# Kernel tuning notes

Measured on AMD Instinct MI355X. Metric: run time of the kernel, lower is better.

## Reference

```python
import jax, jax.numpy as jnp
import numpy as np

B, S, E = 2, 2048, 1024
H, D = 16, 64
BASE = 10000.0


def rotate_half(x):
    x1, x2 = jnp.split(x, 2, axis=-1)
    return jnp.concatenate((-x2, x1), axis=-1)


def rope_cos_sin(seq_len, dim):
    inv_freq = 1.0 / (BASE ** (jnp.arange(0, dim, 2, dtype=jnp.float32) / dim))
    t = jnp.arange(seq_len, dtype=jnp.float32)
    freqs = jnp.einsum('i,j->ij', t, inv_freq)          # [S, D/2]
    emb = jnp.concatenate((freqs, freqs), axis=-1)       # [S, D]
    return jnp.cos(emb), jnp.sin(emb)


def setup_inputs() -> dict:
    key = jax.random.key(0)
    ks = jax.random.split(key, 9)
    s = 1.0 / np.sqrt(E)
    inp = {
        'x': jax.random.normal(ks[0], (B, S, E), dtype=jnp.float32),
        'mask': jnp.ones((B, S), dtype=jnp.int32),
        'Wq': jax.random.normal(ks[1], (E, H * D), dtype=jnp.float32) * s,
        'bq': jnp.zeros((H * D,), dtype=jnp.float32),
        'Wk': jax.random.normal(ks[2], (E, H * D), dtype=jnp.float32) * s,
        'bk': jnp.zeros((H * D,), dtype=jnp.float32),
        'Wv': jax.random.normal(ks[3], (E, H * D), dtype=jnp.float32) * s,
        'bv': jnp.zeros((H * D,), dtype=jnp.float32),
        'Wo': jax.random.normal(ks[4], (H * D, E), dtype=jnp.float32) * s,
        'bo': jnp.zeros((E,), dtype=jnp.float32),
    }
    return inp


def reference(x, mask, Wq, bq, Wk, bk, Wv, bv, Wo, bo):
    b, s, _ = x.shape
    scale = D ** (-0.5)
    # projections -> [B, H, S, D]
    q = (x @ Wq + bq).reshape(b, s, H, D).transpose(0, 2, 1, 3)
    k = (x @ Wk + bk).reshape(b, s, H, D).transpose(0, 2, 1, 3)
    v = (x @ Wv + bv).reshape(b, s, H, D).transpose(0, 2, 1, 3)
    # rotary position embedding
    cos, sin = rope_cos_sin(s, D)                      # [S, D]
    cos = cos[None, None]
    sin = sin[None, None]
    q = q * cos + rotate_half(q) * sin
    k = k * cos + rotate_half(k) * sin
    # scores [B, H, S, S]
    scores = jnp.einsum('bhqd,bhkd->bhqk', q, k) * scale
    # padding mask [B,1,1,S]
    scores = jnp.where(mask[:, None, None, :] == 0, -jnp.inf, scores)
    # causal mask
    i = jnp.arange(s)
    causal = jnp.where(i[None, :] > i[:, None], -jnp.inf, 0.0)  # [S, S]
    scores = scores + causal[None, None]
    attn = jax.nn.softmax(scores, axis=-1)
    ctx = jnp.einsum('bhqk,bhkd->bhqd', attn, v)
    ctx = ctx.transpose(0, 2, 1, 3).reshape(b, s, H * D)
    return ctx @ Wo + bo
```

## Files before the change

### kernel.cpp

```cpp
#include <hip/hip_runtime.h>
#include <cstdint>
#include <cstddef>

#define DEVI __device__ __forceinline__

typedef __bf16 bf16_t;
typedef __bf16 bf16x4 __attribute__((ext_vector_type(4)));
typedef __bf16 bf16x8 __attribute__((ext_vector_type(8)));
typedef float  f32x4  __attribute__((ext_vector_type(4)));
typedef unsigned short u16x4 __attribute__((ext_vector_type(4)));

static constexpr int Bz = 2, S = 2048, E = 1024, H = 16, Dh = 64;
static constexpr int M  = Bz * S;
static constexpr int N  = H * Dh;
static constexpr int Kd = E;

DEVI unsigned short f2bf(float f) {
  unsigned u = __builtin_bit_cast(unsigned, f);
  return (unsigned short)((u + 0x7fffu + ((u >> 16) & 1u)) >> 16);
}

DEVI void async_copy16(void* lds, const void* g) {
  __builtin_amdgcn_global_load_lds((__attribute__((address_space(1))) void*)(g),
                                   (__attribute__((address_space(3))) void*)(lds), 16, 0, 0);
}

__global__ void prep_kernel(const float* __restrict__ x, bf16_t* __restrict__ xb,
                            const float* __restrict__ Wq, const float* __restrict__ Wk,
                            const float* __restrict__ Wv, const float* __restrict__ Wo,
                            bf16_t* __restrict__ WtBase,
                            float* __restrict__ ropeC, float* __restrict__ ropeS) {
  __shared__ unsigned short tile[64][68];
  const int blk = blockIdx.x, tid = threadIdx.x;
  if (blk < 4096) {
    int i = blk * 256 + tid;
    float4 v = ((const float4*)x)[i];
    u16x4 o = { f2bf(v.x), f2bf(v.y), f2bf(v.z), f2bf(v.w) };
    ((u16x4*)xb)[i] = o;
  } else if (blk < 5120) {
    const int i = blk - 4096;
    const int z = i >> 8, rest = i & 255;
    const int n0 = (rest & 15) * 64, k0 = (rest >> 4) * 64;
    const float* W = (z == 0) ? Wq : (z == 1) ? Wk : (z == 2) ? Wv : Wo;
    unsigned short* T = (unsigned short*)(WtBase + (size_t)z * Kd * N);
    for (int e = tid; e < 1024; e += 256) {
      int r = e >> 4, c4 = (e & 15) * 4;
      float4 v = *(const float4*)(W + (size_t)(k0 + r) * N + n0 + c4);
      u16x4 o = { f2bf(v.x), f2bf(v.y), f2bf(v.z), f2bf(v.w) };
      *(u16x4*)&tile[r][c4] = o;
    }
    __syncthreads();
    for (int e = tid; e < 1024; e += 256) {
      int r = e >> 4, c4 = (e & 15) * 4;
      u16x4 o = { tile[c4][r], tile[c4 + 1][r], tile[c4 + 2][r], tile[c4 + 3][r] };
      *(u16x4*)&T[(size_t)(n0 + r) * Kd + k0 + c4] = o;
    }
  } else {
    int i = (blk - 5120) * 256 + tid;
    int pos = i >> 5, j = i & 31;
    float inv = exp2f(-(float)j * 0.41524101186092029f);
    float ang = (float)pos * inv;
    ropeC[i] = cosf(ang);
    ropeS[i] = sinf(ang);
  }
}

__global__ void vtrans_kernel(const bf16_t* __restrict__ V, bf16_t* __restrict__ Vt) {
  __shared__ unsigned short tile[64][68];
  const int bh = blockIdx.y;
  const int s0 = blockIdx.x * 64;
  const unsigned short* Vp = (const unsigned short*)V + (size_t)bh * S * Dh;
  unsigned short* Tp = (unsigned short*)Vt + (size_t)bh * Dh * S;
  const int tid = threadIdx.x;
  for (int e = tid; e < 1024; e += 256) {
    int r = e >> 4, c4 = (e & 15) * 4;
    u16x4 v = *(const u16x4*)(Vp + (size_t)(s0 + r) * Dh + c4);
    *(u16x4*)&tile[r][c4] = v;
  }
  __syncthreads();
  for (int e = tid; e < 1024; e += 256) {
    int d = e >> 4, s4 = (e & 15) * 4;
    u16x4 o = { tile[s4][d], tile[s4 + 1][d], tile[s4 + 2][d], tile[s4 + 3][d] };
    *(u16x4*)&Tp[(size_t)d * S + s0 + s4] = o;
  }
}


DEVI void gemm_mainloop(const bf16_t* __restrict__ A, const bf16_t* __restrict__ Bt,
                        bf16_t* sA, bf16_t* sB, int m0, int n0, f32x4 (&acc)[4][4]) {
  const int tid  = threadIdx.x;
  const int lane = tid & 63;
  const int wid  = tid >> 6;
  const int l16  = lane & 15;
  const int quad = lane >> 4;
  const int wm = (wid >> 1) * 64;
  const int wn = (wid & 1) * 64;
  const int o0 = wid * 2048 + lane * 16;
  const int o1 = o0 + 1024;
  const int r0 = o0 >> 6, c0 = o0 & 63;
  const int r1 = o1 >> 6, c1 = o1 & 63;
  const char* Ab = (const char*)A;
  const char* Bb = (const char*)Bt;
  char* sAc = (char*)sA;
  char* sBc = (char*)sB;

  for (int k0 = 0; k0 < Kd; k0 += 32) {
    __syncthreads();
    async_copy16(sAc + wid * 2048,        Ab + ((size_t)(m0 + r0) * Kd + k0) * 2 + c0);
    async_copy16(sAc + wid * 2048 + 1024, Ab + ((size_t)(m0 + r1) * Kd + k0) * 2 + c1);
    async_copy16(sBc + wid * 2048,        Bb + ((size_t)(n0 + r0) * Kd + k0) * 2 + c0);
    async_copy16(sBc + wid * 2048 + 1024, Bb + ((size_t)(n0 + r1) * Kd + k0) * 2 + c1);
    __syncthreads();
    bf16x8 af[4], bfv[4];
#pragma unroll
    for (int mi = 0; mi < 4; ++mi)
      af[mi] = *(const bf16x8*)(sA + (wm + mi * 16 + l16) * 32 + quad * 8);
#pragma unroll
    for (int ni = 0; ni < 4; ++ni)
      bfv[ni] = *(const bf16x8*)(sB + (wn + ni * 16 + l16) * 32 + quad * 8);
#pragma unroll
    for (int mi = 0; mi < 4; ++mi)
#pragma unroll
      for (int ni = 0; ni < 4; ++ni)
        acc[mi][ni] = __builtin_amdgcn_mfma_f32_16x16x32_bf16(af[mi], bfv[ni], acc[mi][ni], 0, 0, 0);
  }
}

__global__ __launch_bounds__(256, 3) void gemm_qkv_kernel(
    const bf16_t* __restrict__ xb, const bf16_t* __restrict__ WtBase,
    const float* __restrict__ bq, const float* __restrict__ bk, const float* __restrict__ bv,
    bf16_t* __restrict__ outBase,
    const float* __restrict__ ropeC, const float* __restrict__ ropeS) {
  __shared__ bf16_t sA[4096], sB[4096];
  const int z = blockIdx.z;
  const bf16_t* Bt = WtBase + (size_t)z * Kd * N;
  const float* bias = (z == 0) ? bq : (z == 1) ? bk : bv;
  unsigned short* outp = (unsigned short*)(outBase + (size_t)z * M * N);
  const int n0 = blockIdx.x * 128, m0 = blockIdx.y * 128;
  f32x4 acc[4][4] = {};
  gemm_mainloop(xb, Bt, sA, sB, m0, n0, acc);

  const int tid = threadIdx.x, lane = tid & 63, wid = tid >> 6;
  const int l16 = lane & 15, quad = lane >> 4;
  const int wm = (wid >> 1) * 64, wn = (wid & 1) * 64;
  const int cbase = n0 + wn;
  const int h = cbase >> 6;

  if (z < 2) {
    const float qs = (z == 0) ? 0.18033688011112042f : 1.0f;
#pragma unroll
    for (int mi = 0; mi < 4; ++mi)
#pragma unroll
      for (int r = 0; r < 4; ++r) {
        int t = m0 + wm + mi * 16 + quad * 4 + r;
        int bb = t >> 11, s = t & (S - 1);
        size_t obase = ((size_t)(bb * H + h) * S + s) * Dh;
#pragma unroll
        for (int np = 0; np < 2; ++np) {
          int j = np * 16 + l16;
          float cc = ropeC[s * 32 + j];
          float ss = ropeS[s * 32 + j];
          float xlo = acc[mi][np][r]     + bias[cbase + j];
          float xhi = acc[mi][np + 2][r] + bias[cbase + j + 32];
          outp[obase + j]      = f2bf((xlo * cc - xhi * ss) * qs);
          outp[obase + j + 32] = f2bf((xhi * cc + xlo * ss) * qs);
        }
      }
  } else {
#pragma unroll
    for (int mi = 0; mi < 4; ++mi)
#pragma unroll
      for (int r = 0; r < 4; ++r) {
        int t = m0 + wm + mi * 16 + quad * 4 + r;
        int bb = t >> 11, s = t & (S - 1);
        size_t obase = ((size_t)(bb * H + h) * S + s) * Dh;
#pragma unroll
        for (int ni = 0; ni < 4; ++ni) {
          int d = ni * 16 + l16;
          outp[obase + d] = f2bf(acc[mi][ni][r] + bias[cbase + d]);
        }
      }
  }
}

__global__ __launch_bounds__(256, 4) void gemm_o_kernel(
    const bf16_t* __restrict__ A, const bf16_t* __restrict__ Bt,
    const float* __restrict__ bias, float* __restrict__ out) {
  __shared__ bf16_t sA[2048], sB[4096];
  const int n0 = blockIdx.x * 128, m0 = blockIdx.y * 64;
  const int tid = threadIdx.x, lane = tid & 63, wid = tid >> 6;
  const int l16 = lane & 15, quad = lane >> 4;
  const int wm = (wid >> 1) * 32, wn = (wid & 1) * 64;
  const int rowoff = lane >> 2, col8 = (lane & 3) * 8;
  const char* Ab = (const char*)A;
  const char* Bb = (const char*)Bt;
  char* sAc = (char*)sA;
  char* sBc = (char*)sB;
  f32x4 acc[2][4] = {};

  for (int k0 = 0; k0 < Kd; k0 += 32) {
    __syncthreads();
    async_copy16(sAc + wid * 1024,
                 Ab + ((size_t)(m0 + wid * 16 + rowoff) * Kd + k0 + col8) * 2);
    async_copy16(sBc + (wid * 2) * 1024,
                 Bb + ((size_t)(n0 + wid * 32 + rowoff) * Kd + k0 + col8) * 2);
    async_copy16(sBc + (wid * 2 + 1) * 1024,
                 Bb + ((size_t)(n0 + wid * 32 + 16 + rowoff) * Kd + k0 + col8) * 2);
    __syncthreads();
    bf16x8 af[2], bfv[4];
#pragma unroll
    for (int mi = 0; mi < 2; ++mi)
      af[mi] = *(const bf16x8*)(sA + (wm + mi * 16 + l16) * 32 + quad * 8);
#pragma unroll
    for (int ni = 0; ni < 4; ++ni)
      bfv[ni] = *(const bf16x8*)(sB + (wn + ni * 16 + l16) * 32 + quad * 8);
#pragma unroll
    for (int mi = 0; mi < 2; ++mi)
#pragma unroll
      for (int ni = 0; ni < 4; ++ni)
        acc[mi][ni] = __builtin_amdgcn_mfma_f32_16x16x32_bf16(af[mi], bfv[ni], acc[mi][ni], 0, 0, 0);
  }
#pragma unroll
  for (int mi = 0; mi < 2; ++mi)
#pragma unroll
    for (int r = 0; r < 4; ++r) {
      int t = m0 + wm + mi * 16 + quad * 4 + r;
#pragma unroll
      for (int ni = 0; ni < 4; ++ni) {
        int c = n0 + wn + ni * 16 + l16;
        out[(size_t)t * N + c] = acc[mi][ni][r] + bias[c];
      }
    }
}

__global__ __launch_bounds__(256, 3) void attn_kernel(
    const bf16_t* __restrict__ Q, const bf16_t* __restrict__ Kb,
    const bf16_t* __restrict__ Vt, const int* __restrict__ mask,
    bf16_t* __restrict__ ctx) {
  __shared__ bf16_t sK[8192];
  __shared__ bf16_t sV[8192];
  __shared__ unsigned short sP[4][16 * 136];

  const int tid = threadIdx.x, lane = tid & 63, wid = tid >> 6;
  const int l16 = lane & 15, quad = lane >> 4;

  const int idx = blockIdx.x;
  const int qb  = 31 - (idx >> 5);
  const int bh  = idx & 31;
  const int b   = bh >> 4;
  const int q0  = qb * 64;
  const int qw  = q0 + wid * 16;

  const bf16_t* Qp = Q + ((size_t)bh * S + qw) * Dh;
  const char*   Kg = (const char*)(Kb + (size_t)bh * S * Dh);
  const char*   Vg = (const char*)(Vt + (size_t)bh * Dh * S);
  const int*    mp = mask + b * S;

  bf16x8 qf0 = *(const bf16x8*)(Qp + l16 * Dh + quad * 8);
  bf16x8 qf1 = *(const bf16x8*)(Qp + l16 * Dh + 32 + quad * 8);

  int    sLds[4];
  size_t kGo[4], vGo[4];
#pragma unroll
  for (int i = 0; i < 4; ++i) {
    int sk = wid * 4 + i;
    int g = sk >> 1, c = sk & 1;
    sLds[i] = sk * 1024;
    kGo[i] = ((size_t)(g * 16 + l16) * Dh + c * 32 + quad * 8) * 2;
    vGo[i] = ((size_t)(wid * 16 + l16) * S + i * 32 + quad * 8) * 2;
  }
  char* sKc = (char*)sK;
  char* sVc = (char*)sV;

  f32x4 acc[4] = {};
  float lsum = 0.f;
  const int qcol = qw + l16;
  const int niter = (qb >> 1) + 1;
  unsigned short* pb = &sP[wid][0];

  for (int kt = 0; kt < niter; ++kt) {
    const int kb = kt * 128;
    __syncthreads();
#pragma unroll
    for (int i = 0; i < 4; ++i) {
      async_copy16(sKc + sLds[i], Kg + (size_t)kb * (Dh * 2) + kGo[i]);
      async_copy16(sVc + sLds[i], Vg + (size_t)kb * 2 + vGo[i]);
    }
    int mk0 = mp[kb + lane];
    int mk1 = mp[kb + 64 + lane];
    __syncthreads();

    f32x4 st[8];
#pragma unroll
    for (int g = 0; g < 8; ++g) {
      bf16x8 kf0 = *(const bf16x8*)(sK + (g * 2 + 0) * 512 + lane * 8);
      bf16x8 kf1 = *(const bf16x8*)(sK + (g * 2 + 1) * 512 + lane * 8);
      f32x4 z = {};
      z = __builtin_amdgcn_mfma_f32_16x16x32_bf16(kf0, qf0, z, 0, 0, 0);
      z = __builtin_amdgcn_mfma_f32_16x16x32_bf16(kf1, qf1, z, 0, 0, 0);
      st[g] = z;
    }

    unsigned long long dm0 = __ballot(mk0 == 0);
    unsigned long long dm1 = __ballot(mk1 == 0);
    if (dm0 | dm1) {
#pragma unroll
      for (int g = 0; g < 8; ++g) {
        unsigned long long dm = (g < 4) ? dm0 : dm1;
#pragma unroll
        for (int r = 0; r < 4; ++r)
          if ((dm >> ((g & 3) * 16 + quad * 4 + r)) & 1ull) st[g][r] = -1e30f;
      }
    }
    if (kt == niter - 1) {
#pragma unroll
      for (int g = 0; g < 8; ++g)
#pragma unroll
        for (int r = 0; r < 4; ++r)
          if (kb + g * 16 + quad * 4 + r > qcol) st[g][r] = -1e30f;
    }

#pragma unroll
    for (int g = 0; g < 8; ++g) {
      float e0 = exp2f(st[g][0]), e1 = exp2f(st[g][1]);
      float e2 = exp2f(st[g][2]), e3 = exp2f(st[g][3]);
      lsum += (e0 + e1) + (e2 + e3);
      bf16x4 pk = { (bf16_t)e0, (bf16_t)e1, (bf16_t)e2, (bf16_t)e3 };
      *(bf16x4*)&pb[l16 * 136 + g * 16 + quad * 4] = pk;
    }
    bf16x8 pf[4];
#pragma unroll
    for (int kc = 0; kc < 4; ++kc)
      pf[kc] = *(const bf16x8*)((const bf16_t*)(const void*)pb + l16 * 136 + kc * 32 + quad * 8);

#pragma unroll
    for (int dt = 0; dt < 4; ++dt)
#pragma unroll
      for (int kc = 0; kc < 4; ++kc) {
        bf16x8 vf = *(const bf16x8*)(sV + (dt * 4 + kc) * 512 + lane * 8);
        acc[dt] = __builtin_amdgcn_mfma_f32_16x16x32_bf16(vf, pf[kc], acc[dt], 0, 0, 0);
      }
  }

  lsum += __shfl_xor(lsum, 16);
  lsum += __shfl_xor(lsum, 32);
  float inv = 1.0f / lsum;
  unsigned short* cp = (unsigned short*)ctx;
  size_t trow = ((size_t)(b * S + qw + l16)) * N + (size_t)(bh & 15) * Dh;
#pragma unroll
  for (int dt = 0; dt < 4; ++dt) {
    u16x4 o = { f2bf(acc[dt][0] * inv), f2bf(acc[dt][1] * inv),
                f2bf(acc[dt][2] * inv), f2bf(acc[dt][3] * inv) };
    *(u16x4*)&cp[trow + dt * 16 + quad * 4] = o;
  }
}


extern "C" void kernel_launch(void* const* d_in, const int* in_sizes, int n_in,
                              void* d_out, int out_size, void* d_ws, size_t ws_size,
                              hipStream_t stream) {
  const float* x  = (const float*)d_in[0];
  const int*  msk = (const int*)d_in[1];
  const float* Wq = (const float*)d_in[2];
  const float* bq = (const float*)d_in[3];
  const float* Wk = (const float*)d_in[4];
  const float* bk = (const float*)d_in[5];
  const float* Wv = (const float*)d_in[6];
  const float* bv = (const float*)d_in[7];
  const float* Wo = (const float*)d_in[8];
  const float* bo = (const float*)d_in[9];
  float* out = (float*)d_out;
  (void)in_sizes; (void)n_in; (void)out_size; (void)ws_size;

  char* ws = (char*)d_ws;
  bf16_t* xb   = (bf16_t*)(ws);
  bf16_t* WT   = (bf16_t*)(ws + (8u  << 20));
  bf16_t* qkv  = (bf16_t*)(ws + (16u << 20));
  bf16_t* Qb   = qkv;
  bf16_t* Kbuf = qkv + (size_t)1 * M * N;
  bf16_t* Vb   = qkv + (size_t)2 * M * N;
  bf16_t* Vt   = xb;
  bf16_t* ctx  = Vb;
  float* ropeC = (float*)(ws + (40u << 20));
  float* ropeS = ropeC + (size_t)S * 32;

  prep_kernel<<<5376, 256, 0, stream>>>(x, xb, Wq, Wk, Wv, Wo, WT, ropeC, ropeS);
  gemm_qkv_kernel<<<dim3(8, 32, 3), 256, 0, stream>>>(xb, WT, bq, bk, bv, qkv, ropeC, ropeS);
  vtrans_kernel<<<dim3(32, 32), 256, 0, stream>>>(Vb, Vt);
  attn_kernel<<<1024, 256, 0, stream>>>(Qb, Kbuf, Vt, msk, ctx);
  gemm_o_kernel<<<dim3(8, 64), 256, 0, stream>>>(ctx, WT + (size_t)3 * Kd * N, bo, out);
}
```

Before: 197.8 us.

## Pair causal query blocks per CTA with double-buffered K/V and mask fast path

Each attention block now handles two query tiles (j and 31-j) that share K/V tiles, which balances causal work and halves the grid. K/V loads are double-buffered with explicit vmcnt waits and raw barriers, so the next tile's global-to-LDS copy overlaps compute. A one-time mask scan chooses a template path that skips per-tile mask loads and ballots when no positions are padded. It also adds an XOR swizzle on the P scratch buffer and setprio around MFMA sections. In exchange, LDS use doubles and occupancy drops to 2 blocks per CU.

After: 204.1 us. 3.2% more time.

```diff
diff --git a/kernel.cpp b/kernel.cpp
--- a/kernel.cpp
+++ b/kernel.cpp
@@ -24,6 +24,9 @@
   __builtin_amdgcn_global_load_lds((__attribute__((address_space(1))) void*)(g),
                                    (__attribute__((address_space(3))) void*)(lds), 16, 0, 0);
 }
+
+#define VMCNT8() asm volatile("s_waitcnt vmcnt(8)" ::: "memory")
+#define VMCNT0() asm volatile("s_waitcnt vmcnt(0)" ::: "memory")
 
 __global__ void prep_kernel(const float* __restrict__ x, bf16_t* __restrict__ xb,
                             const float* __restrict__ Wq, const float* __restrict__ Wk,
@@ -233,126 +236,220 @@
     }
 }
 
-__global__ __launch_bounds__(256, 3) void attn_kernel(
+template <bool MASKED>
+DEVI void attn_body(const bf16_t* __restrict__ Qp, const char* __restrict__ Kg,
+                    const char* __restrict__ Vg, const int* __restrict__ mp,
+                    unsigned short* __restrict__ cp, char* sKc, char* sVc,
+                    unsigned short* __restrict__ pb, int b, int bh,
+                    int qbS, int qbL) {
+  const int tid = threadIdx.x, lane = tid & 63, wid = tid >> 6;
+  const int l16 = lane & 15, quad = lane >> 4;
+  const int nS = (qbS >> 1) + 1, nL = (qbL >> 1) + 1;
+  const int qwS = qbS * 64 + wid * 16, qwL = qbL * 64 + wid * 16;
+  const int qcS = qwS + l16, qcL = qwL + l16;
+  const int swz = (l16 & 7) << 4;
+
+  bf16x8 qSf0 = *(const bf16x8*)(Qp + (size_t)(qwS + l16) * Dh + quad * 8);
+  bf16x8 qSf1 = *(const bf16x8*)(Qp + (size_t)(qwS + l16) * Dh + 32 + quad * 8);
+  bf16x8 qLf0 = *(const bf16x8*)(Qp + (size_t)(qwL + l16) * Dh + quad * 8);
+  bf16x8 qLf1 = *(const bf16x8*)(Qp + (size_t)(qwL + l16) * Dh + 32 + quad * 8);
+
+  int sLds[4], kGo[4], vGo[4];
+#pragma unroll
+  for (int i = 0; i < 4; ++i) {
+    int sk = wid * 4 + i, g = sk >> 1, c = sk & 1;
+    sLds[i] = sk * 1024;
+    kGo[i] = ((g * 16 + l16) * Dh + c * 32 + quad * 8) * 2;
+    vGo[i] = ((wid * 16 + l16) * S + i * 32 + quad * 8) * 2;
+  }
+
+  f32x4 accL[4] = {}, accS[4] = {};
+  float lsumL = 0.f, lsumS = 0.f;
+
+#pragma unroll
+  for (int i = 0; i < 4; ++i) {
+    async_copy16(sKc + sLds[i], Kg + kGo[i]);
+    async_copy16(sVc + sLds[i], Vg + vGo[i]);
+  }
+
+  for (int kt = 0; kt < nL; ++kt) {
+    const int cur = kt & 1;
+    const int kb = kt * 128;
+    if (kt + 1 < nL) {
+      const char* Kn = Kg + (size_t)(kb + 128) * (Dh * 2);
+      const char* Vn = Vg + (size_t)(kb + 128) * 2;
+      char* kd = sKc + (cur ^ 1) * 16384;
+      char* vd = sVc + (cur ^ 1) * 16384;
+#pragma unroll
+      for (int i = 0; i < 4; ++i) {
+        async_copy16(kd + sLds[i], Kn + kGo[i]);
+        async_copy16(vd + sLds[i], Vn + vGo[i]);
+      }
+      if (!MASKED) { VMCNT8(); }
+    } else if (!MASKED) {
+      VMCNT0();
+    }
+    int mk0 = 0, mk1 = 0;
+    if (MASKED) {
+      mk0 = mp[kb + lane];
+      mk1 = mp[kb + 64 + lane];
+      VMCNT0();
+    }
+    __builtin_amdgcn_s_barrier();
+
+    const bf16_t* sKt = (const bf16_t*)(sKc + cur * 16384);
+    const bf16_t* sVt = (const bf16_t*)(sVc + cur * 16384);
+    const bool doS = kt < nS;
+
+    f32x4 stL[8], stS[8];
+    __builtin_amdgcn_s_setprio(1);
+#pragma unroll
+    for (int g = 0; g < 8; ++g) {
+      bf16x8 kf0 = *(const bf16x8*)(sKt + (g * 2 + 0) * 512 + lane * 8);
+      bf16x8 kf1 = *(const bf16x8*)(sKt + (g * 2 + 1) * 512 + lane * 8);
+      f32x4 z = {};
+      z = __builtin_amdgcn_mfma_f32_16x16x32_bf16(kf0, qLf0, z, 0, 0, 0);
+      z = __builtin_amdgcn_mfma_f32_16x16x32_bf16(kf1, qLf1, z, 0, 0, 0);
+      stL[g] = z;
+      if (doS) {
+        f32x4 y = {};
+        y = __builtin_amdgcn_mfma_f32_16x16x32_bf16(kf0, qSf0, y, 0, 0, 0);
+        y = __builtin_amdgcn_mfma_f32_16x16x32_bf16(kf1, qSf1, y, 0, 0, 0);
+        stS[g] = y;
+      }
+    }
+    __builtin_amdgcn_s_setprio(0);
+
+    if (MASKED) {
+      unsigned long long dm0 = __ballot(mk0 == 0);
+      unsigned long long dm1 = __ballot(mk1 == 0);
+      if (dm0 | dm1) {
+#pragma unroll
+        for (int g = 0; g < 8; ++g) {
+          unsigned long long dm = (g < 4) ? dm0 : dm1;
+#pragma unroll
+          for (int r = 0; r < 4; ++r)
+            if ((dm >> ((g & 3) * 16 + quad * 4 + r)) & 1ull) {
+              stL[g][r] = -1e30f;
+              if (doS) stS[g][r] = -1e30f;
+            }
+        }
+      }
+    }
+    if (kt == nL - 1) {
+#pragma unroll
+      for (int g = 0; g < 8; ++g)
+#pragma unroll
+        for (int r = 0; r < 4; ++r)
+          if (kb + g * 16 + quad * 4 + r > qcL) stL[g][r] = -1e30f;
+    }
+    if (doS && kt == nS - 1) {
+#pragma unroll
+      for (int g = 0; g < 8; ++g)
+#pragma unroll
+        for (int r = 0; r < 4; ++r)
+          if (kb + g * 16 + quad * 4 + r > qcS) stS[g][r] = -1e30f;
+    }
+
+#pragma unroll
+    for (int g = 0; g < 8; ++g) {
+      float e0 = exp2f(stL[g][0]), e1 = exp2f(stL[g][1]);
+      float e2 = exp2f(stL[g][2]), e3 = exp2f(stL[g][3]);
+      lsumL += (e0 + e1) + (e2 + e3);
+      bf16x4 pk = { (bf16_t)e0, (bf16_t)e1, (bf16_t)e2, (bf16_t)e3 };
+      *(bf16x4*)((char*)pb + ((l16 * 256 + g * 32 + quad * 8) ^ swz)) = pk;
+    }
+    {
+      bf16x8 pf[4];
+#pragma unroll
+      for (int kc = 0; kc < 4; ++kc)
+        pf[kc] = *(const bf16x8*)((const char*)pb + ((l16 * 256 + kc * 64 + quad * 16) ^ swz));
+      __builtin_amdgcn_s_setprio(1);
+#pragma unroll
+      for (int dt = 0; dt < 4; ++dt)
+#pragma unroll
+        for (int kc = 0; kc < 4; ++kc) {
+          bf16x8 vf = *(const bf16x8*)(sVt + (dt * 4 + kc) * 512 + lane * 8);
+          accL[dt] = __builtin_amdgcn_mfma_f32_16x16x32_bf16(vf, pf[kc], accL[dt], 0, 0, 0);
+        }
+      __builtin_amdgcn_s_setprio(0);
+    }
+    if (doS) {
+#pragma unroll
+      for (int g = 0; g < 8; ++g) {
+        float e0 = exp2f(stS[g][0]), e1 = exp2f(stS[g][1]);
+        float e2 = exp2f(stS[g][2]), e3 = exp2f(stS[g][3]);
+        lsumS += (e0 + e1) + (e2 + e3);
+        bf16x4 pk = { (bf16_t)e0, (bf16_t)e1, (bf16_t)e2, (bf16_t)e3 };
+        *(bf16x4*)((char*)pb + ((l16 * 256 + g * 32 + quad * 8) ^ swz)) = pk;
+      }
+      bf16x8 pf[4];
+#pragma unroll
+      for (int kc = 0; kc < 4; ++kc)
+        pf[kc] = *(const bf16x8*)((const char*)pb + ((l16 * 256 + kc * 64 + quad * 16) ^ swz));
+      __builtin_amdgcn_s_setprio(1);
+#pragma unroll
+      for (int dt = 0; dt < 4; ++dt)
+#pragma unroll
+        for (int kc = 0; kc < 4; ++kc) {
+          bf16x8 vf = *(const bf16x8*)(sVt + (dt * 4 + kc) * 512 + lane * 8);
+          accS[dt] = __builtin_amdgcn_mfma_f32_16x16x32_bf16(vf, pf[kc], accS[dt], 0, 0, 0);
+        }
+      __builtin_amdgcn_s_setprio(0);
+    }
+    __builtin_amdgcn_s_barrier();
+  }
+
+  lsumL += __shfl_xor(lsumL, 16); lsumL += __shfl_xor(lsumL, 32);
+  lsumS += __shfl_xor(lsumS, 16); lsumS += __shfl_xor(lsumS, 32);
+  const float invL = 1.0f / lsumL, invS = 1.0f / lsumS;
+  const size_t trL = ((size_t)(b * S + qwL + l16)) * N + (size_t)(bh & 15) * Dh;
+  const size_t trS = ((size_t)(b * S + qwS + l16)) * N + (size_t)(bh & 15) * Dh;
+#pragma unroll
+  for (int dt = 0; dt < 4; ++dt) {
+    u16x4 oL = { f2bf(accL[dt][0] * invL), f2bf(accL[dt][1] * invL),
+                 f2bf(accL[dt][2] * invL), f2bf(accL[dt][3] * invL) };
+    *(u16x4*)&cp[trL + dt * 16 + quad * 4] = oL;
+    u16x4 oS = { f2bf(accS[dt][0] * invS), f2bf(accS[dt][1] * invS),
+                 f2bf(accS[dt][2] * invS), f2bf(accS[dt][3] * invS) };
+    *(u16x4*)&cp[trS + dt * 16 + quad * 4] = oS;
+  }
+}
+
+__global__ __launch_bounds__(256, 2) void attn_kernel(
     const bf16_t* __restrict__ Q, const bf16_t* __restrict__ Kb,
     const bf16_t* __restrict__ Vt, const int* __restrict__ mask,
     bf16_t* __restrict__ ctx) {
-  __shared__ bf16_t sK[8192];
-  __shared__ bf16_t sV[8192];
-  __shared__ unsigned short sP[4][16 * 136];
-
-  const int tid = threadIdx.x, lane = tid & 63, wid = tid >> 6;
-  const int l16 = lane & 15, quad = lane >> 4;
+  __shared__ bf16_t sK[2][8192];
+  __shared__ bf16_t sV[2][8192];
+  __shared__ unsigned short sP[4][2048];
 
   const int idx = blockIdx.x;
-  const int qb  = 31 - (idx >> 5);
-  const int bh  = idx & 31;
-  const int b   = bh >> 4;
-  const int q0  = qb * 64;
-  const int qw  = q0 + wid * 16;
-
-  const bf16_t* Qp = Q + ((size_t)bh * S + qw) * Dh;
+  const int j  = idx >> 5;
+  const int bh = idx & 31;
+  const int b  = bh >> 4;
+  const int lane = threadIdx.x & 63, wid = threadIdx.x >> 6;
+
+  const bf16_t* Qp = Q + (size_t)bh * S * Dh;
   const char*   Kg = (const char*)(Kb + (size_t)bh * S * Dh);
   const char*   Vg = (const char*)(Vt + (size_t)bh * Dh * S);
   const int*    mp = mask + b * S;
 
-  bf16x8 qf0 = *(const bf16x8*)(Qp + l16 * Dh + quad * 8);
-  bf16x8 qf1 = *(const bf16x8*)(Qp + l16 * Dh + 32 + quad * 8);
-
-  int    sLds[4];
-  size_t kGo[4], vGo[4];
-#pragma unroll
-  for (int i = 0; i < 4; ++i) {
-    int sk = wid * 4 + i;
-    int g = sk >> 1, c = sk & 1;
-    sLds[i] = sk * 1024;
-    kGo[i] = ((size_t)(g * 16 + l16) * Dh + c * 32 + quad * 8) * 2;
-    vGo[i] = ((size_t)(wid * 16 + l16) * S + i * 32 + quad * 8) * 2;
-  }
-  char* sKc = (char*)sK;
-  char* sVc = (char*)sV;
-
-  f32x4 acc[4] = {};
-  float lsum = 0.f;
-  const int qcol = qw + l16;
-  const int niter = (qb >> 1) + 1;
-  unsigned short* pb = &sP[wid][0];
-
-  for (int kt = 0; kt < niter; ++kt) {
-    const int kb = kt * 128;
-    __syncthreads();
-#pragma unroll
-    for (int i = 0; i < 4; ++i) {
-      async_copy16(sKc + sLds[i], Kg + (size_t)kb * (Dh * 2) + kGo[i]);
-      async_copy16(sVc + sLds[i], Vg + (size_t)kb * 2 + vGo[i]);
-    }
-    int mk0 = mp[kb + lane];
-    int mk1 = mp[kb + 64 + lane];
-    __syncthreads();
-
-    f32x4 st[8];
-#pragma unroll
-    for (int g = 0; g < 8; ++g) {
-      bf16x8 kf0 = *(const bf16x8*)(sK + (g * 2 + 0) * 512 + lane * 8);
-      bf16x8 kf1 = *(const bf16x8*)(sK + (g * 2 + 1) * 512 + lane * 8);
-      f32x4 z = {};
-      z = __builtin_amdgcn_mfma_f32_16x16x32_bf16(kf0, qf0, z, 0, 0, 0);
-      z = __builtin_amdgcn_mfma_f32_16x16x32_bf16(kf1, qf1, z, 0, 0, 0);
-      st[g] = z;
-    }
-
-    unsigned long long dm0 = __ballot(mk0 == 0);
-    unsigned long long dm1 = __ballot(mk1 == 0);
-    if (dm0 | dm1) {
-#pragma unroll
-      for (int g = 0; g < 8; ++g) {
-        unsigned long long dm = (g < 4) ? dm0 : dm1;
-#pragma unroll
-        for (int r = 0; r < 4; ++r)
-          if ((dm >> ((g & 3) * 16 + quad * 4 + r)) & 1ull) st[g][r] = -1e30f;
-      }
-    }
-    if (kt == niter - 1) {
-#pragma unroll
-      for (int g = 0; g < 8; ++g)
-#pragma unroll
-        for (int r = 0; r < 4; ++r)
-          if (kb + g * 16 + quad * 4 + r > qcol) st[g][r] = -1e30f;
-    }
-
-#pragma unroll
-    for (int g = 0; g < 8; ++g) {
-      float e0 = exp2f(st[g][0]), e1 = exp2f(st[g][1]);
-      float e2 = exp2f(st[g][2]), e3 = exp2f(st[g][3]);
-      lsum += (e0 + e1) + (e2 + e3);
-      bf16x4 pk = { (bf16_t)e0, (bf16_t)e1, (bf16_t)e2, (bf16_t)e3 };
-      *(bf16x4*)&pb[l16 * 136 + g * 16 + quad * 4] = pk;
-    }
-    bf16x8 pf[4];
-#pragma unroll
-    for (int kc = 0; kc < 4; ++kc)
-      pf[kc] = *(const bf16x8*)((const bf16_t*)(const void*)pb + l16 * 136 + kc * 32 + quad * 8);
-
-#pragma unroll
-    for (int dt = 0; dt < 4; ++dt)
-#pragma unroll
-      for (int kc = 0; kc < 4; ++kc) {
-        bf16x8 vf = *(const bf16x8*)(sV + (dt * 4 + kc) * 512 + lane * 8);
-        acc[dt] = __builtin_amdgcn_mfma_f32_16x16x32_bf16(vf, pf[kc], acc[dt], 0, 0, 0);
-      }
-  }
-
-  lsum += __shfl_xor(lsum, 16);
-  lsum += __shfl_xor(lsum, 32);
-  float inv = 1.0f / lsum;
+  int dead = 0;
+  const int4* mp4 = (const int4*)mp;
+  for (int c = lane; c < S / 4; c += 64) {
+    int4 m = mp4[c];
+    dead |= (m.x == 0) | (m.y == 0) | (m.z == 0) | (m.w == 0);
+  }
+  const bool anydead = __ballot(dead != 0) != 0ull;
+
   unsigned short* cp = (unsigned short*)ctx;
-  size_t trow = ((size_t)(b * S + qw + l16)) * N + (size_t)(bh & 15) * Dh;
-#pragma unroll
-  for (int dt = 0; dt < 4; ++dt) {
-    u16x4 o = { f2bf(acc[dt][0] * inv), f2bf(acc[dt][1] * inv),
-                f2bf(acc[dt][2] * inv), f2bf(acc[dt][3] * inv) };
-    *(u16x4*)&cp[trow + dt * 16 + quad * 4] = o;
-  }
+  if (!anydead)
+    attn_body<false>(Qp, Kg, Vg, mp, cp, (char*)&sK[0][0], (char*)&sV[0][0],
+                     &sP[wid][0], b, bh, j, 31 - j);
+  else
+    attn_body<true>(Qp, Kg, Vg, mp, cp, (char*)&sK[0][0], (char*)&sV[0][0],
+                    &sP[wid][0], b, bh, j, 31 - j);
 }
 
 
@@ -387,6 +484,6 @@
   prep_kernel<<<5376, 256, 0, stream>>>(x, xb, Wq, Wk, Wv, Wo, WT, ropeC, ropeS);
   gemm_qkv_kernel<<<dim3(8, 32, 3), 256, 0, stream>>>(xb, WT, bq, bk, bv, qkv, ropeC, ropeS);
   vtrans_kernel<<<dim3(32, 32), 256, 0, stream>>>(Vb, Vt);
-  attn_kernel<<<1024, 256, 0, stream>>>(Qb, Kbuf, Vt, msk, ctx);
+  attn_kernel<<<512, 256, 0, stream>>>(Qb, Kbuf, Vt, msk, ctx);
   gemm_o_kernel<<<dim3(8, 64), 256, 0, stream>>>(ctx, WT + (size_t)3 * Kd * N, bo, out);
 }
```

## Rewrite attention with 32x32 MFMA, split-K warp groups and double-buffered K/V

Applied to the files above, without the earlier changes.

The attention kernel now runs 512-thread blocks over 128-query tiles, split into two warp groups that each cover half of the key range and combine their partial sums through LDS at the end. It uses 32x32x16 MFMAs and builds the P operand in registers with cvt_pk and permlane32 swaps instead of a round trip through LDS. K/V tiles are double-buffered with async global-to-LDS copies. A block-wide mask precheck selects a template path that skips per-tile mask loads when nothing is masked. The scheduling is more complex and raises register/LDS pressure, and the query tiles are ordered to balance causal work.

Measured after the change: 196.1 us. Within noise of the previous version (-0.8%).

```diff
diff --git a/kernel.cpp b/kernel.cpp
--- a/kernel.cpp
+++ b/kernel.cpp
@@ -8,7 +8,9 @@
 typedef __bf16 bf16x4 __attribute__((ext_vector_type(4)));
 typedef __bf16 bf16x8 __attribute__((ext_vector_type(8)));
 typedef float  f32x4  __attribute__((ext_vector_type(4)));
+typedef float  f32x16 __attribute__((ext_vector_type(16)));
 typedef unsigned short u16x4 __attribute__((ext_vector_type(4)));
+typedef unsigned int   u32x4 __attribute__((ext_vector_type(4)));
 
 static constexpr int Bz = 2, S = 2048, E = 1024, H = 16, Dh = 64;
 static constexpr int M  = Bz * S;
@@ -23,6 +25,19 @@
 DEVI void async_copy16(void* lds, const void* g) {
   __builtin_amdgcn_global_load_lds((__attribute__((address_space(1))) void*)(g),
                                    (__attribute__((address_space(3))) void*)(lds), 16, 0, 0);
+}
+
+DEVI void block_sync() { asm volatile("s_barrier" ::: "memory"); }
+#define VMCNT4() asm volatile("s_waitcnt vmcnt(4)" ::: "memory")
+#define VMCNT0() asm volatile("s_waitcnt vmcnt(0)" ::: "memory")
+
+DEVI unsigned cvtpk(float lo, float hi) {
+  unsigned r;
+  asm("v_cvt_pk_bf16_f32 %0, %1, %2" : "=v"(r) : "v"(lo), "v"(hi));
+  return r;
+}
+DEVI void swap32(unsigned& x, unsigned& y) {
+  asm("v_permlane32_swap_b32 %0, %1" : "+v"(x), "+v"(y));
 }
 
 __global__ void prep_kernel(const float* __restrict__ x, bf16_t* __restrict__ xb,
@@ -233,126 +248,192 @@
     }
 }
 
-__global__ __launch_bounds__(256, 3) void attn_kernel(
+template <bool MASKED>
+DEVI void attn32_body(const bf16_t* __restrict__ Qp, const char* __restrict__ Kg,
+                      const char* __restrict__ Vg, const int* __restrict__ mp,
+                      unsigned short* __restrict__ cp, char* lds,
+                      int b, int bh, int qb) {
+  const int tid = threadIdx.x, lane = tid & 63, wid = tid >> 6;
+  const int grp = wid >> 2, w4 = wid & 3;
+  const int l32 = lane & 31, hi = lane >> 5;
+
+  const int qw = qb * 128 + w4 * 32;
+  const int qg = qw + l32;
+  const int nIt = qb + 1;
+  const int gk0 = grp * nIt * 64;
+  char* gB = lds + grp * 32768;
+
+  bf16x8 qf[4];
+#pragma unroll
+  for (int c = 0; c < 4; ++c)
+    qf[c] = *(const bf16x8*)(Qp + (size_t)(qw + l32) * Dh + c * 16 + hi * 8);
+  asm volatile("" :: "v"((float)qf[3][7]));
+
+  int kLds[2], vLds[2], kOff[2], vOff[2];
+#pragma unroll
+  for (int i = 0; i < 2; ++i) {
+    const int s = w4 * 2 + i;
+    const int a = s >> 2, c = s & 3;
+    kLds[i] = s * 1024;
+    kOff[i] = ((a * 32 + l32) * Dh + c * 16 + hi * 8) * 2;
+    vLds[i] = 8192 + s * 1024;
+    vOff[i] = ((s >> 2) * 32 + l32) * (S * 2) + (((s & 3) * 16 + hi * 8) * 2);
+  }
+
+  f32x16 cacc0 = {}, cacc1 = {};
+  float lsum = 0.f;
+
+  {
+    const char* ks = Kg + (size_t)gk0 * (Dh * 2);
+    const char* vs = Vg + (size_t)gk0 * 2;
+    async_copy16(gB + kLds[0], ks + kOff[0]);
+    async_copy16(gB + kLds[1], ks + kOff[1]);
+    async_copy16(gB + vLds[0], vs + vOff[0]);
+    async_copy16(gB + vLds[1], vs + vOff[1]);
+  }
+
+  for (int kt = 0; kt < nIt; ++kt) {
+    const int cur = kt & 1;
+    const int kb = gk0 + kt * 64;
+    if (kt + 1 < nIt) {
+      char* dst = gB + (cur ^ 1) * 16384;
+      const char* ks = Kg + (size_t)(kb + 64) * (Dh * 2);
+      const char* vs = Vg + (size_t)(kb + 64) * 2;
+      async_copy16(dst + kLds[0], ks + kOff[0]);
+      async_copy16(dst + kLds[1], ks + kOff[1]);
+      async_copy16(dst + vLds[0], vs + vOff[0]);
+      async_copy16(dst + vLds[1], vs + vOff[1]);
+      if (!MASKED) { VMCNT4(); }
+    } else if (!MASKED) {
+      VMCNT0();
+    }
+    unsigned long long dm = 0;
+    if (MASKED) {
+      int mk = mp[kb + lane];
+      VMCNT0();
+      dm = __ballot(mk == 0);
+    }
+    block_sync();
+
+    const bf16_t* sK = (const bf16_t*)(gB + cur * 16384);
+    const bf16_t* sV = (const bf16_t*)(gB + cur * 16384 + 8192);
+    const bool needC = (kb + 63 > qw);
+
+#pragma unroll
+    for (int a = 0; a < 2; ++a) {
+      f32x16 st = {};
+      __builtin_amdgcn_s_setprio(1);
+#pragma unroll
+      for (int c = 0; c < 4; ++c) {
+        bf16x8 kf = *(const bf16x8*)(sK + (a * 4 + c) * 512 + lane * 8);
+        st = __builtin_amdgcn_mfma_f32_32x32x16_bf16(kf, qf[c], st, 0, 0, 0);
+      }
+      __builtin_amdgcn_s_setprio(0);
+      if (MASKED && dm) {
+#pragma unroll
+        for (int r = 0; r < 16; ++r)
+          if ((dm >> (a * 32 + (r & 3) + 8 * (r >> 2) + 4 * hi)) & 1ull) st[r] = -1e30f;
+      }
+      if (needC) {
+        const int kbase = kb + a * 32 + 4 * hi - qg;
+#pragma unroll
+        for (int r = 0; r < 16; ++r)
+          if (kbase + (r & 3) + 8 * (r >> 2) > 0) st[r] = -1e30f;
+      }
+      unsigned P0[4], P1[4];
+#pragma unroll
+      for (int m = 0; m < 4; ++m) {
+        float p0 = exp2f(st[4 * m + 0]), p1 = exp2f(st[4 * m + 1]);
+        float p2 = exp2f(st[4 * m + 2]), p3 = exp2f(st[4 * m + 3]);
+        lsum += (p0 + p1) + (p2 + p3);
+        P0[m] = cvtpk(p0, p1);
+        P1[m] = cvtpk(p2, p3);
+      }
+      swap32(P0[0], P0[1]); swap32(P1[0], P1[1]);
+      swap32(P0[2], P0[3]); swap32(P1[2], P1[3]);
+      u32x4 t0 = { P0[0], P1[0], P0[1], P1[1] };
+      u32x4 t1 = { P0[2], P1[2], P0[3], P1[3] };
+      const bf16x8 f0 = __builtin_bit_cast(bf16x8, t0);
+      const bf16x8 f1 = __builtin_bit_cast(bf16x8, t1);
+      __builtin_amdgcn_s_setprio(1);
+      {
+        bf16x8 v00 = *(const bf16x8*)(sV + (0 + a * 2 + 0) * 512 + lane * 8);
+        cacc0 = __builtin_amdgcn_mfma_f32_32x32x16_bf16(v00, f0, cacc0, 0, 0, 0);
+        bf16x8 v01 = *(const bf16x8*)(sV + (0 + a * 2 + 1) * 512 + lane * 8);
+        cacc0 = __builtin_amdgcn_mfma_f32_32x32x16_bf16(v01, f1, cacc0, 0, 0, 0);
+        bf16x8 v10 = *(const bf16x8*)(sV + (4 + a * 2 + 0) * 512 + lane * 8);
+        cacc1 = __builtin_amdgcn_mfma_f32_32x32x16_bf16(v10, f0, cacc1, 0, 0, 0);
+        bf16x8 v11 = *(const bf16x8*)(sV + (4 + a * 2 + 1) * 512 + lane * 8);
+        cacc1 = __builtin_amdgcn_mfma_f32_32x32x16_bf16(v11, f1, cacc1, 0, 0, 0);
+      }
+      __builtin_amdgcn_s_setprio(0);
+    }
+    block_sync();
+  }
+
+  float* cm = (float*)lds + (size_t)w4 * 2112;
+  if (grp == 1) {
+#pragma unroll
+    for (int r = 0; r < 16; ++r) cm[r * 64 + lane] = cacc0[r];
+#pragma unroll
+    for (int r = 0; r < 16; ++r) cm[(16 + r) * 64 + lane] = cacc1[r];
+    cm[2048 + lane] = lsum;
+  }
+  asm volatile("s_waitcnt lgkmcnt(0)" ::: "memory");
+  block_sync();
+  if (grp == 0) {
+#pragma unroll
+    for (int r = 0; r < 16; ++r) cacc0[r] += cm[r * 64 + lane];
+#pragma unroll
+    for (int r = 0; r < 16; ++r) cacc1[r] += cm[(16 + r) * 64 + lane];
+    lsum += cm[2048 + lane];
+    lsum += __shfl_xor(lsum, 32);
+    const float inv = 1.0f / lsum;
+    const size_t base = ((size_t)(b * S + qw + l32)) * N + (size_t)(bh & 15) * Dh;
+#pragma unroll
+    for (int m = 0; m < 4; ++m) {
+      const int d0 = m * 8 + 4 * hi;
+      u16x4 o0 = { f2bf(cacc0[4 * m + 0] * inv), f2bf(cacc0[4 * m + 1] * inv),
+                   f2bf(cacc0[4 * m + 2] * inv), f2bf(cacc0[4 * m + 3] * inv) };
+      *(u16x4*)&cp[base + d0] = o0;
+      u16x4 o1 = { f2bf(cacc1[4 * m + 0] * inv), f2bf(cacc1[4 * m + 1] * inv),
+                   f2bf(cacc1[4 * m + 2] * inv), f2bf(cacc1[4 * m + 3] * inv) };
+      *(u16x4*)&cp[base + 32 + d0] = o1;
+    }
+  }
+}
+
+__global__ __launch_bounds__(512, 4) void attn_kernel(
     const bf16_t* __restrict__ Q, const bf16_t* __restrict__ Kb,
     const bf16_t* __restrict__ Vt, const int* __restrict__ mask,
     bf16_t* __restrict__ ctx) {
-  __shared__ bf16_t sK[8192];
-  __shared__ bf16_t sV[8192];
-  __shared__ unsigned short sP[4][16 * 136];
-
-  const int tid = threadIdx.x, lane = tid & 63, wid = tid >> 6;
-  const int l16 = lane & 15, quad = lane >> 4;
+  __shared__ f32x4 ldsA[4096];
 
   const int idx = blockIdx.x;
-  const int qb  = 31 - (idx >> 5);
-  const int bh  = idx & 31;
-  const int b   = bh >> 4;
-  const int q0  = qb * 64;
-  const int qw  = q0 + wid * 16;
-
-  const bf16_t* Qp = Q + ((size_t)bh * S + qw) * Dh;
+  const int g  = idx >> 5;
+  const int bh = idx & 31;
+  const int qb = (g < 8) ? (15 - g) : (g - 8);
+  const int b  = bh >> 4;
+  const int lane = threadIdx.x & 63;
+
+  const bf16_t* Qp = Q + (size_t)bh * S * Dh;
   const char*   Kg = (const char*)(Kb + (size_t)bh * S * Dh);
   const char*   Vg = (const char*)(Vt + (size_t)bh * Dh * S);
   const int*    mp = mask + b * S;
 
-  bf16x8 qf0 = *(const bf16x8*)(Qp + l16 * Dh + quad * 8);
-  bf16x8 qf1 = *(const bf16x8*)(Qp + l16 * Dh + 32 + quad * 8);
-
-  int    sLds[4];
-  size_t kGo[4], vGo[4];
-#pragma unroll
-  for (int i = 0; i < 4; ++i) {
-    int sk = wid * 4 + i;
-    int g = sk >> 1, c = sk & 1;
-    sLds[i] = sk * 1024;
-    kGo[i] = ((size_t)(g * 16 + l16) * Dh + c * 32 + quad * 8) * 2;
-    vGo[i] = ((size_t)(wid * 16 + l16) * S + i * 32 + quad * 8) * 2;
-  }
-  char* sKc = (char*)sK;
-  char* sVc = (char*)sV;
-
-  f32x4 acc[4] = {};
-  float lsum = 0.f;
-  const int qcol = qw + l16;
-  const int niter = (qb >> 1) + 1;
-  unsigned short* pb = &sP[wid][0];
-
-  for (int kt = 0; kt < niter; ++kt) {
-    const int kb = kt * 128;
-    __syncthreads();
-#pragma unroll
-    for (int i = 0; i < 4; ++i) {
-      async_copy16(sKc + sLds[i], Kg + (size_t)kb * (Dh * 2) + kGo[i]);
-      async_copy16(sVc + sLds[i], Vg + (size_t)kb * 2 + vGo[i]);
-    }
-    int mk0 = mp[kb + lane];
-    int mk1 = mp[kb + 64 + lane];
-    __syncthreads();
-
-    f32x4 st[8];
-#pragma unroll
-    for (int g = 0; g < 8; ++g) {
-      bf16x8 kf0 = *(const bf16x8*)(sK + (g * 2 + 0) * 512 + lane * 8);
-      bf16x8 kf1 = *(const bf16x8*)(sK + (g * 2 + 1) * 512 + lane * 8);
-      f32x4 z = {};
-      z = __builtin_amdgcn_mfma_f32_16x16x32_bf16(kf0, qf0, z, 0, 0, 0);
-      z = __builtin_amdgcn_mfma_f32_16x16x32_bf16(kf1, qf1, z, 0, 0, 0);
-      st[g] = z;
-    }
-
-    unsigned long long dm0 = __ballot(mk0 == 0);
-    unsigned long long dm1 = __ballot(mk1 == 0);
-    if (dm0 | dm1) {
-#pragma unroll
-      for (int g = 0; g < 8; ++g) {
-        unsigned long long dm = (g < 4) ? dm0 : dm1;
-#pragma unroll
-        for (int r = 0; r < 4; ++r)
-          if ((dm >> ((g & 3) * 16 + quad * 4 + r)) & 1ull) st[g][r] = -1e30f;
-      }
-    }
-    if (kt == niter - 1) {
-#pragma unroll
-      for (int g = 0; g < 8; ++g)
-#pragma unroll
-        for (int r = 0; r < 4; ++r)
-          if (kb + g * 16 + quad * 4 + r > qcol) st[g][r] = -1e30f;
-    }
-
-#pragma unroll
-    for (int g = 0; g < 8; ++g) {
-      float e0 = exp2f(st[g][0]), e1 = exp2f(st[g][1]);
-      float e2 = exp2f(st[g][2]), e3 = exp2f(st[g][3]);
-      lsum += (e0 + e1) + (e2 + e3);
-      bf16x4 pk = { (bf16_t)e0, (bf16_t)e1, (bf16_t)e2, (bf16_t)e3 };
-      *(bf16x4*)&pb[l16 * 136 + g * 16 + quad * 4] = pk;
-    }
-    bf16x8 pf[4];
-#pragma unroll
-    for (int kc = 0; kc < 4; ++kc)
-      pf[kc] = *(const bf16x8*)((const bf16_t*)(const void*)pb + l16 * 136 + kc * 32 + quad * 8);
-
-#pragma unroll
-    for (int dt = 0; dt < 4; ++dt)
-#pragma unroll
-      for (int kc = 0; kc < 4; ++kc) {
-        bf16x8 vf = *(const bf16x8*)(sV + (dt * 4 + kc) * 512 + lane * 8);
-        acc[dt] = __builtin_amdgcn_mfma_f32_16x16x32_bf16(vf, pf[kc], acc[dt], 0, 0, 0);
-      }
-  }
-
-  lsum += __shfl_xor(lsum, 16);
-  lsum += __shfl_xor(lsum, 32);
-  float inv = 1.0f / lsum;
+  int dead = 0;
+  const int4* mp4 = (const int4*)mp;
+  for (int c = lane; c < S / 4; c += 64) {
+    int4 m = mp4[c];
+    dead |= (m.x == 0) | (m.y == 0) | (m.z == 0) | (m.w == 0);
+  }
+  const bool anydead = __ballot(dead != 0) != 0ull;
+
   unsigned short* cp = (unsigned short*)ctx;
-  size_t trow = ((size_t)(b * S + qw + l16)) * N + (size_t)(bh & 15) * Dh;
-#pragma unroll
-  for (int dt = 0; dt < 4; ++dt) {
-    u16x4 o = { f2bf(acc[dt][0] * inv), f2bf(acc[dt][1] * inv),
-                f2bf(acc[dt][2] * inv), f2bf(acc[dt][3] * inv) };
-    *(u16x4*)&cp[trow + dt * 16 + quad * 4] = o;
-  }
+  if (!anydead)
+    attn32_body<false>(Qp, Kg, Vg, mp, cp, (char*)ldsA, b, bh, qb);
+  else
+    attn32_body<true>(Qp, Kg, Vg, mp, cp, (char*)ldsA, b, bh, qb);
 }
 
 
@@ -387,6 +468,6 @@
   prep_kernel<<<5376, 256, 0, stream>>>(x, xb, Wq, Wk, Wv, Wo, WT, ropeC, ropeS);
   gemm_qkv_kernel<<<dim3(8, 32, 3), 256, 0, stream>>>(xb, WT, bq, bk, bv, qkv, ropeC, ropeS);
   vtrans_kernel<<<dim3(32, 32), 256, 0, stream>>>(Vb, Vt);
-  attn_kernel<<<1024, 256, 0, stream>>>(Qb, Kbuf, Vt, msk, ctx);
+  attn_kernel<<<512, 512, 0, stream>>>(Qb, Kbuf, Vt, msk, ctx);
   gemm_o_kernel<<<dim3(8, 64), 256, 0, stream>>>(ctx, WT + (size_t)3 * Kd * N, bo, out);
 }
```
